# Kernel optimization log

Hardware: AMD Instinct MI355X
Metric: run time of the kernel (lower is better)

## Reference

```python
import jax, jax.numpy as jnp
import numpy as np

D_MODEL, STATE_DIM = 256, 16
BATCH, SEQLEN = 8, 2048


def setup_inputs() -> dict:
    key = jax.random.key(0)
    k1, k2, k3, k4, k5 = jax.random.split(key, 5)
    x = jax.random.normal(k1, (BATCH, SEQLEN, D_MODEL), dtype=jnp.float32)
    # A is parameterized as -exp(randn) in the torch module's init
    A = -jnp.exp(jax.random.normal(k2, (D_MODEL, STATE_DIM), dtype=jnp.float32))
    B = jax.random.normal(k3, (D_MODEL, STATE_DIM), dtype=jnp.float32)
    C = jax.random.normal(k4, (D_MODEL, STATE_DIM), dtype=jnp.float32)
    D = jnp.ones((D_MODEL,), dtype=jnp.float32)
    delta = jax.random.uniform(k5, (D_MODEL,), dtype=jnp.float32) * 0.1 + 0.001
    return {"x": x, "A": A, "B": B, "C": C, "D": D, "delta": delta}


def reference(x, A, B, C, D, delta):
    # x: (Bsz, L, D_model); A,B,C: (D_model, N); D,delta: (D_model,)
    dt = jax.nn.sigmoid(delta)[:, None]          # (D, 1)
    A_bar = jnp.exp(dt * A)                      # (D, N), time-invariant
    B_bar = dt * B                               # (D, N)

    def step(h, x_t):
        # h: (Bsz, D, N); x_t: (Bsz, D)
        h = A_bar[None] * h + B_bar[None] * x_t[:, :, None]
        y_t = jnp.einsum('bdn,dn->bd', h, C)
        return h, y_t

    h0 = jnp.zeros((x.shape[0], x.shape[2], A.shape[1]), dtype=x.dtype)
    _, ys = jax.lax.scan(step, h0, jnp.swapaxes(x, 0, 1))  # ys: (L, Bsz, D)
    y = jnp.swapaxes(ys, 0, 1)                   # (Bsz, L, D)
    return y + x * D[None, None, :]
```

## Files before the change

kernel.cpp:

```cpp
#include <hip/hip_runtime.h>

#define BSZ  8
#define LSEQ 2048
#define DM   256
#define NS   16
#define NC   64
#define LC   (LSEQ/NC)
#define TILE_FLOATS (LC * DM)
#define VEC_ROUNDS  (TILE_FLOATS / 4 / DM)

__global__ void k_local(
        const float* __restrict__ x,
        const float* __restrict__ A,
        const float* __restrict__ Bm,
        const float* __restrict__ delta,
        float* __restrict__ carry) {
    __shared__ float lx[TILE_FLOATS];
    const int d     = threadIdx.x;
    const int chunk = blockIdx.x & (NC - 1);
    const int b     = blockIdx.x / NC;

    {
        const float4* __restrict__ src =
            (const float4*)(x + ((size_t)(b * LSEQ + chunk * LC)) * DM);
        float4* dst = (float4*)lx;
#pragma unroll
        for (int r = 0; r < VEC_ROUNDS; ++r)
            dst[r * DM + d] = src[r * DM + d];
    }

    const float dt = 1.0f / (1.0f + expf(-delta[d]));
    float a[NS], bb[NS];
#pragma unroll
    for (int n = 0; n < NS; ++n) {
        a[n]  = expf(dt * A[d * NS + n]);
        bb[n] = dt * Bm[d * NS + n];
    }
    __syncthreads();

    float h[NS];
#pragma unroll
    for (int n = 0; n < NS; ++n) h[n] = 0.0f;
#pragma unroll 4
    for (int t = 0; t < LC; ++t) {
        const float xv = lx[t * DM + d];
#pragma unroll
        for (int n = 0; n < NS; ++n) h[n] = fmaf(a[n], h[n], bb[n] * xv);
    }

    float* cp = carry + ((size_t)(b * NC + chunk) * NS) * DM + d;
#pragma unroll
    for (int n = 0; n < NS; ++n) cp[(size_t)n * DM] = h[n];
}

__global__ void k_prefix(
        const float* __restrict__ A,
        const float* __restrict__ delta,
        float* __restrict__ carry) {
    const int tid = blockIdx.x * 256 + threadIdx.x;
    const int d = tid & (DM - 1);
    const int n = (tid >> 8) & (NS - 1);
    const int b = tid >> 12;

    const float dt = 1.0f / (1.0f + expf(-delta[d]));
    const float aL = expf(dt * A[d * NS + n] * (float)LC);

    float* cp = carry + (size_t)b * NC * NS * DM + (size_t)n * DM + d;

    float v[NC];
#pragma unroll
    for (int j = 0; j < NC; ++j) v[j] = cp[(size_t)j * NS * DM];

    float run = 0.0f;
#pragma unroll
    for (int j = 0; j < NC; ++j) {
        const float c = v[j];
        v[j] = run;
        run = fmaf(aL, run, c);
    }

#pragma unroll
    for (int j = 0; j < NC; ++j) cp[(size_t)j * NS * DM] = v[j];
}

__global__ void k_final(
        const float* __restrict__ x,
        const float* __restrict__ A,
        const float* __restrict__ Bm,
        const float* __restrict__ Cm,
        const float* __restrict__ Dv,
        const float* __restrict__ delta,
        const float* __restrict__ hin,
        float* __restrict__ y) {
    __shared__ float lt[TILE_FLOATS];
    const int d     = threadIdx.x;
    const int chunk = blockIdx.x & (NC - 1);
    const int b     = blockIdx.x / NC;

    float h[NS];
    const float* hp = hin + ((size_t)(b * NC + chunk) * NS) * DM + d;
#pragma unroll
    for (int n = 0; n < NS; ++n) h[n] = hp[(size_t)n * DM];

    const size_t tile_base = ((size_t)(b * LSEQ + chunk * LC)) * DM;
    {
        const float4* __restrict__ src = (const float4*)(x + tile_base);
        float4* dst = (float4*)lt;
#pragma unroll
        for (int r = 0; r < VEC_ROUNDS; ++r)
            dst[r * DM + d] = src[r * DM + d];
    }

    const float dt = 1.0f / (1.0f + expf(-delta[d]));
    float a[NS], bb[NS], cc[NS];
#pragma unroll
    for (int n = 0; n < NS; ++n) {
        a[n]  = expf(dt * A[d * NS + n]);
        bb[n] = dt * Bm[d * NS + n];
        cc[n] = Cm[d * NS + n];
    }
    const float Dd = Dv[d];
    __syncthreads();

#pragma unroll 4
    for (int t = 0; t < LC; ++t) {
        const float xv = lt[t * DM + d];
        float acc = Dd * xv;
#pragma unroll
        for (int n = 0; n < NS; ++n) {
            h[n] = fmaf(a[n], h[n], bb[n] * xv);
            acc  = fmaf(h[n], cc[n], acc);
        }
        lt[t * DM + d] = acc;
    }
    __syncthreads();

    {
        float4* __restrict__ dst = (float4*)(y + tile_base);
        const float4* src = (const float4*)lt;
#pragma unroll
        for (int r = 0; r < VEC_ROUNDS; ++r)
            dst[r * DM + d] = src[r * DM + d];
    }
}

extern "C" void kernel_launch(void* const* d_in, const int* in_sizes, int n_in,
                              void* d_out, int out_size, void* d_ws, size_t ws_size,
                              hipStream_t stream) {
    const float* x     = (const float*)d_in[0];
    const float* A     = (const float*)d_in[1];
    const float* Bm    = (const float*)d_in[2];
    const float* Cm    = (const float*)d_in[3];
    const float* Dv    = (const float*)d_in[4];
    const float* delta = (const float*)d_in[5];
    float* y = (float*)d_out;

    float* carry = (float*)d_ws;

    dim3 blk(DM);
    dim3 grd1(BSZ * NC);
    k_local<<<grd1, blk, 0, stream>>>(x, A, Bm, delta, carry);

    dim3 grd2((BSZ * NS * DM) / 256);
    k_prefix<<<grd2, dim3(256), 0, stream>>>(A, delta, carry);

    k_final<<<grd1, blk, 0, stream>>>(x, A, Bm, Cm, Dv, delta, carry, y);
}
```

Measured before the change: 32.34 us.

## Halve chunk count and split channels across two 128-thread blocks

Cuts the number of sequence chunks from 64 to 32, which doubles the chunk length, and splits the 256 channels into two halves, each handled by its own 128-thread block. The local-carry kernel now reads x directly from global memory instead of staging it in shared memory. The final kernel stages only a half-width tile, using coalesced float4 row segments. This shortens the serial prefix scan and shrinks the carry buffer and LDS use. In exchange, each thread runs twice as many serial recurrence steps and fewer total threads are in flight.

```diff
diff --git a/kernel.cpp b/kernel.cpp
--- a/kernel.cpp
+++ b/kernel.cpp
@@ -4,10 +4,11 @@
 #define LSEQ 2048
 #define DM   256
 #define NS   16
-#define NC   64
+#define NC   32
 #define LC   (LSEQ/NC)
-#define TILE_FLOATS (LC * DM)
-#define VEC_ROUNDS  (TILE_FLOATS / 4 / DM)
+#define DH   128
+#define TPB  DH
+#define HALF_FLOATS (LC * DH)
 
 __global__ void k_local(
         const float* __restrict__ x,
@@ -15,19 +16,11 @@
         const float* __restrict__ Bm,
         const float* __restrict__ delta,
         float* __restrict__ carry) {
-    __shared__ float lx[TILE_FLOATS];
-    const int d     = threadIdx.x;
-    const int chunk = blockIdx.x & (NC - 1);
-    const int b     = blockIdx.x / NC;
-
-    {
-        const float4* __restrict__ src =
-            (const float4*)(x + ((size_t)(b * LSEQ + chunk * LC)) * DM);
-        float4* dst = (float4*)lx;
-#pragma unroll
-        for (int r = 0; r < VEC_ROUNDS; ++r)
-            dst[r * DM + d] = src[r * DM + d];
-    }
+    const int i     = threadIdx.x;
+    const int dh    = blockIdx.x & 1;
+    const int chunk = (blockIdx.x >> 1) & (NC - 1);
+    const int b     = blockIdx.x >> 6;
+    const int d     = dh * DH + i;
 
     const float dt = 1.0f / (1.0f + expf(-delta[d]));
     float a[NS], bb[NS];
@@ -36,14 +29,15 @@
         a[n]  = expf(dt * A[d * NS + n]);
         bb[n] = dt * Bm[d * NS + n];
     }
-    __syncthreads();
 
     float h[NS];
 #pragma unroll
     for (int n = 0; n < NS; ++n) h[n] = 0.0f;
+
+    const float* xp = x + ((size_t)(b * LSEQ + chunk * LC)) * DM + d;
 #pragma unroll 4
     for (int t = 0; t < LC; ++t) {
-        const float xv = lx[t * DM + d];
+        const float xv = xp[(size_t)t * DM];
 #pragma unroll
         for (int n = 0; n < NS; ++n) h[n] = fmaf(a[n], h[n], bb[n] * xv);
     }
@@ -92,10 +86,12 @@
         const float* __restrict__ delta,
         const float* __restrict__ hin,
         float* __restrict__ y) {
-    __shared__ float lt[TILE_FLOATS];
-    const int d     = threadIdx.x;
-    const int chunk = blockIdx.x & (NC - 1);
-    const int b     = blockIdx.x / NC;
+    __shared__ float lt[HALF_FLOATS];
+    const int i     = threadIdx.x;
+    const int dh    = blockIdx.x & 1;
+    const int chunk = (blockIdx.x >> 1) & (NC - 1);
+    const int b     = blockIdx.x >> 6;
+    const int d     = dh * DH + i;
 
     float h[NS];
     const float* hp = hin + ((size_t)(b * NC + chunk) * NS) * DM + d;
@@ -103,12 +99,16 @@
     for (int n = 0; n < NS; ++n) h[n] = hp[(size_t)n * DM];
 
     const size_t tile_base = ((size_t)(b * LSEQ + chunk * LC)) * DM;
+    const float* src_base = x + tile_base + dh * DH;
     {
-        const float4* __restrict__ src = (const float4*)(x + tile_base);
-        float4* dst = (float4*)lt;
+        float4* lt4 = (float4*)lt;
 #pragma unroll
-        for (int r = 0; r < VEC_ROUNDS; ++r)
-            dst[r * DM + d] = src[r * DM + d];
+        for (int r = 0; r < 16; ++r) {
+            const int t  = r * 4 + (i >> 5);
+            const int c4 = i & 31;
+            lt4[r * DH + i] =
+                ((const float4*)(src_base + (size_t)t * DM))[c4];
+        }
     }
 
     const float dt = 1.0f / (1.0f + expf(-delta[d]));
@@ -124,23 +124,26 @@
 
 #pragma unroll 4
     for (int t = 0; t < LC; ++t) {
-        const float xv = lt[t * DM + d];
+        const float xv = lt[t * DH + i];
         float acc = Dd * xv;
 #pragma unroll
         for (int n = 0; n < NS; ++n) {
             h[n] = fmaf(a[n], h[n], bb[n] * xv);
             acc  = fmaf(h[n], cc[n], acc);
         }
-        lt[t * DM + d] = acc;
+        lt[t * DH + i] = acc;
     }
     __syncthreads();
 
     {
-        float4* __restrict__ dst = (float4*)(y + tile_base);
-        const float4* src = (const float4*)lt;
+        float* dst_base = y + tile_base + dh * DH;
+        const float4* lt4 = (const float4*)lt;
 #pragma unroll
-        for (int r = 0; r < VEC_ROUNDS; ++r)
-            dst[r * DM + d] = src[r * DM + d];
+        for (int r = 0; r < 16; ++r) {
+            const int t  = r * 4 + (i >> 5);
+            const int c4 = i & 31;
+            ((float4*)(dst_base + (size_t)t * DM))[c4] = lt4[r * DH + i];
+        }
     }
 }
 
@@ -157,12 +160,11 @@
 
     float* carry = (float*)d_ws;
 
-    dim3 blk(DM);
-    dim3 grd1(BSZ * NC);
-    k_local<<<grd1, blk, 0, stream>>>(x, A, Bm, delta, carry);
+    dim3 grd1(BSZ * NC * 2);
+    k_local<<<grd1, dim3(TPB), 0, stream>>>(x, A, Bm, delta, carry);
 
     dim3 grd2((BSZ * NS * DM) / 256);
     k_prefix<<<grd2, dim3(256), 0, stream>>>(A, delta, carry);
 
-    k_final<<<grd1, blk, 0, stream>>>(x, A, Bm, Cm, Dv, delta, carry, y);
+    k_final<<<grd1, dim3(TPB), 0, stream>>>(x, A, Bm, Cm, Dv, delta, carry, y);
 }
```

After: 33.54 us. +3.7%, slower.
